# Kernel optimization log

Measured on AMD Instinct MI355X. Metric: run time of the kernel, lower is better.

## Reference

```python
import jax, jax.numpy as jnp
import numpy as np

NUM_HEADS = 12


def setup_inputs() -> dict:
    key = jax.random.key(0)
    k1, k2, k3, k4 = jax.random.split(key, 4)
    B, N, C = 8, 1024, 768
    x = jax.random.normal(k1, (B, N, C), dtype=jnp.float32)
    # nn.Linear(dim, 3*dim, bias=False): weight applied as x @ W, shape [C, 3C]
    w_qkv = jax.random.normal(k2, (C, 3 * C), dtype=jnp.float32) * (C ** -0.5)
    # nn.Linear(dim, dim) with bias
    w_proj = jax.random.normal(k3, (C, C), dtype=jnp.float32) * (C ** -0.5)
    b_proj = jax.random.normal(k4, (C,), dtype=jnp.float32) * 0.01
    return {"x": x, "w_qkv": w_qkv, "w_proj": w_proj, "b_proj": b_proj, "H": 32, "W": 32}


def reference(x, w_qkv, w_proj, b_proj, H, W):
    B, N, C = x.shape
    nh = NUM_HEADS
    hd = C // nh
    scale = hd ** -0.5
    qkv = (x @ w_qkv).reshape(B, N, 3, nh, hd)
    q, k, v = jnp.moveaxis(qkv, 2, 0)  # each [B, N, nh, hd]
    attn = jnp.einsum("bnhd,bmhd->bhnm", q, k) * scale  # [B, nh, N, N]
    attn = jax.nn.softmax(attn, axis=-1)
    out = jnp.einsum("bhnm,bmhd->bnhd", attn, v).reshape(B, N, C)
    return out @ w_proj + b_proj
```

## Files before the change

kernel.cpp:

```cpp
#include <hip/hip_runtime.h>

typedef __bf16 bf16x8 __attribute__((ext_vector_type(8)));
typedef float f32x4 __attribute__((ext_vector_type(4)));
typedef float f32x16 __attribute__((ext_vector_type(16)));
typedef unsigned short u16;
typedef unsigned int u32;
typedef u16 u16x4 __attribute__((ext_vector_type(4)));
typedef u32 u32x4 __attribute__((ext_vector_type(4)));

__device__ __forceinline__ u16 f2bf(float f) {
    union { float f; u32 u; } x{f};
    u32 r = x.u + 0x7FFFu + ((x.u >> 16) & 1u);
    return (u16)(r >> 16);
}

__device__ __forceinline__ float ex2(float x) {
#if __has_builtin(__builtin_amdgcn_exp2f)
    return __builtin_amdgcn_exp2f(x);
#else
    return __expf(x * 0.6931471805599453f);
#endif
}

__device__ __forceinline__ u32 pkbf(float a, float b) {
    union { float f; u32 u; } ca{a}, cb{b};
    return ((ca.u + 0x8000u) >> 16) | (((cb.u + 0x8000u) >> 16) << 16);
}

#define GLD16(g, l)                                                            \
    __builtin_amdgcn_global_load_lds(                                          \
        (const __attribute__((address_space(1))) u32*)(g),                     \
        (__attribute__((address_space(3))) u32*)(l), 16, 0, 0)

__global__ void convert_bf16(const float* __restrict__ src, u16* __restrict__ dst, int n4) {
    int i = blockIdx.x * blockDim.x + threadIdx.x;
    if (i < n4) {
        float4 f = *(const float4*)(src + (size_t)i * 4);
        u16x4 u = { f2bf(f.x), f2bf(f.y), f2bf(f.z), f2bf(f.w) };
        *(u16x4*)(dst + (size_t)i * 4) = u;
    }
}

__global__ __launch_bounds__(256) void prep_weights(
    const float* __restrict__ wq, const float* __restrict__ wp,
    u16* __restrict__ WqT, u16* __restrict__ WpT)
{
    __shared__ u16 tile[32][33];
    int id = blockIdx.x;
    const float* src; u16* dst; int R, C, bx, by;
    if (id < 1728) { src = wq; dst = WqT; R = 768; C = 2304; bx = (id % 72) * 32; by = (id / 72) * 32; }
    else { id -= 1728; src = wp; dst = WpT; R = 768; C = 768; bx = (id % 24) * 32; by = (id / 24) * 32; }
    int x = threadIdx.x & 31, y = threadIdx.x >> 5;
    #pragma unroll
    for (int i = 0; i < 32; i += 8)
        tile[y + i][x] = f2bf(src[(size_t)(by + y + i) * C + bx + x]);
    __syncthreads();
    #pragma unroll
    for (int i = 0; i < 32; i += 8)
        dst[(size_t)(bx + y + i) * R + by + x] = tile[x][y + i];
}

template <int K>
__global__ __launch_bounds__(256) void gemm_qkv(
    const u16* __restrict__ A,
    const u16* __restrict__ Wt,
    u16* __restrict__ QKV,
    u16* __restrict__ Vt,
    float qscale)
{
    __shared__ __align__(16) u16 As[128 * 64];
    __shared__ __align__(16) u16 Bs[128 * 64];

    int tid = threadIdx.x;
    int wave = tid >> 6, lane = tid & 63;
    int quad = lane >> 4, l16 = lane & 15;
    int wm = (wave >> 1) * 64, wn = (wave & 1) * 64;
    int bm = blockIdx.y * 128, bn = blockIdx.x * 128;
    bool vsec = (bn >= 1536);

    f32x4 acc[4][4] = {};

    int srow = lane >> 3;
    int scg = ((lane & 7) ^ srow) * 8;
    const u16* Ap = A + (size_t)(bm + wave * 32 + srow) * K + scg;
    const u16* Bp = Wt + (size_t)(bn + wave * 32 + srow) * K + scg;

    int fg0 = (((0 * 4 + quad) ^ (l16 & 7)) * 8);
    int fg1 = (((1 * 4 + quad) ^ (l16 & 7)) * 8);

    for (int k0 = 0; k0 < K; k0 += 64) {
        #pragma unroll
        for (int j = 0; j < 4; j++) {
            GLD16(Ap + k0 + (size_t)j * 8 * K, &As[(wave * 32 + j * 8) * 64]);
            GLD16(Bp + k0 + (size_t)j * 8 * K, &Bs[(wave * 32 + j * 8) * 64]);
        }
        __syncthreads();

        #pragma unroll
        for (int h = 0; h < 2; h++) {
            int fg = h ? fg1 : fg0;
            bf16x8 af[4], bfr[4];
            #pragma unroll
            for (int i = 0; i < 4; i++) {
                af[i]  = *(const bf16x8*)&As[(wm + i * 16 + l16) * 64 + fg];
                bfr[i] = *(const bf16x8*)&Bs[(wn + i * 16 + l16) * 64 + fg];
            }
            if (!vsec) {
                #pragma unroll
                for (int mi = 0; mi < 4; mi++)
                    #pragma unroll
                    for (int ni = 0; ni < 4; ni++)
                        acc[mi][ni] = __builtin_amdgcn_mfma_f32_16x16x32_bf16(af[mi], bfr[ni], acc[mi][ni], 0, 0, 0);
            } else {
                #pragma unroll
                for (int mi = 0; mi < 4; mi++)
                    #pragma unroll
                    for (int ni = 0; ni < 4; ni++)
                        acc[mi][ni] = __builtin_amdgcn_mfma_f32_16x16x32_bf16(bfr[ni], af[mi], acc[mi][ni], 0, 0, 0);
            }
        }
        __syncthreads();
    }

    if (!vsec) {
        #pragma unroll
        for (int mi = 0; mi < 4; mi++) {
            #pragma unroll
            for (int ni = 0; ni < 4; ni++) {
                #pragma unroll
                for (int rg = 0; rg < 4; rg++) {
                    int row = bm + wm + mi * 16 + quad * 4 + rg;
                    int col = bn + wn + ni * 16 + l16;
                    float sc = (col < 768) ? qscale : 1.0f;
                    QKV[(size_t)row * 2304 + col] = f2bf(acc[mi][ni][rg] * sc);
                }
            }
        }
    } else {
        #pragma unroll
        for (int mi = 0; mi < 4; mi++) {
            #pragma unroll
            for (int ni = 0; ni < 4; ni++) {
                #pragma unroll
                for (int rg = 0; rg < 4; rg++) {
                    int d = (bn - 1536) + wn + ni * 16 + quad * 4 + rg;
                    int ng = bm + wm + mi * 16 + l16;
                    int b = ng >> 10, n = ng & 1023, h = d >> 6;
                    Vt[((size_t)(b * 12 + h) * 64 + (d & 63)) * 1024 + n] = f2bf(acc[mi][ni][rg]);
                }
            }
        }
    }
}

template <int K>
__global__ __launch_bounds__(256) void gemm_proj(
    const u16* __restrict__ A,
    const u16* __restrict__ Bt,
    float* __restrict__ Cp,
    const float* __restrict__ bias,
    int M, int N)
{
    __shared__ __align__(16) u16 As[128 * 64];
    __shared__ __align__(16) u16 Bs[128 * 64];

    int tid = threadIdx.x;
    int wave = tid >> 6, lane = tid & 63;
    int quad = lane >> 4, l16 = lane & 15;
    int wm = (wave >> 1) * 64, wn = (wave & 1) * 64;
    int bm = blockIdx.y * 128, bn = blockIdx.x * 128;

    f32x4 acc[4][4] = {};

    int srow = lane >> 3;
    int scg = ((lane & 7) ^ srow) * 8;
    const u16* Ap = A + (size_t)(bm + wave * 32 + srow) * K + scg;
    const u16* Bp = Bt + (size_t)(bn + wave * 32 + srow) * K + scg;

    int fg0 = (((0 * 4 + quad) ^ (l16 & 7)) * 8);
    int fg1 = (((1 * 4 + quad) ^ (l16 & 7)) * 8);

    for (int k0 = 0; k0 < K; k0 += 64) {
        #pragma unroll
        for (int j = 0; j < 4; j++) {
            GLD16(Ap + k0 + (size_t)j * 8 * K, &As[(wave * 32 + j * 8) * 64]);
            GLD16(Bp + k0 + (size_t)j * 8 * K, &Bs[(wave * 32 + j * 8) * 64]);
        }
        __syncthreads();

        #pragma unroll
        for (int h = 0; h < 2; h++) {
            int fg = h ? fg1 : fg0;
            bf16x8 af[4], bfr[4];
            #pragma unroll
            for (int i = 0; i < 4; i++) {
                af[i]  = *(const bf16x8*)&As[(wm + i * 16 + l16) * 64 + fg];
                bfr[i] = *(const bf16x8*)&Bs[(wn + i * 16 + l16) * 64 + fg];
            }
            #pragma unroll
            for (int mi = 0; mi < 4; mi++)
                #pragma unroll
                for (int ni = 0; ni < 4; ni++)
                    acc[mi][ni] = __builtin_amdgcn_mfma_f32_16x16x32_bf16(af[mi], bfr[ni], acc[mi][ni], 0, 0, 0);
        }
        __syncthreads();
    }

    #pragma unroll
    for (int mi = 0; mi < 4; mi++) {
        #pragma unroll
        for (int ni = 0; ni < 4; ni++) {
            #pragma unroll
            for (int rg = 0; rg < 4; rg++) {
                int row = bm + wm + mi * 16 + quad * 4 + rg;
                int col = bn + wn + ni * 16 + l16;
                Cp[(size_t)row * N + col] = acc[mi][ni][rg] + bias[col];
            }
        }
    }
}

__global__ __launch_bounds__(256, 4) void attn_kernel(
    const u16* __restrict__ qkv,
    const u16* __restrict__ Vt,
    u16* __restrict__ ctx)
{
    __shared__ __align__(16) u16 Ks[2][4096];
    __shared__ __align__(16) u16 Vs[2][4096];

    int qt = blockIdx.x;
    int bh = blockIdx.y;
    int b = bh / 12, h = bh % 12;
    int tid = threadIdx.x;
    int wave = tid >> 6, lane = tid & 63;
    int l32 = lane & 31, half = lane >> 5;

    const u16* qbase = qkv + (size_t)(b * 1024 + qt * 128 + wave * 32 + l32) * 2304 + h * 64;
    bf16x8 qa[4];
    #pragma unroll
    for (int ks = 0; ks < 4; ks++)
        qa[ks] = *(const bf16x8*)(qbase + ks * 16 + half * 8);

    int srow = lane >> 3;
    int scol = (lane & 7) ^ srow;
    const u16* kA = qkv + (size_t)(b * 1024 + wave * 16 + srow) * 2304 + 768 + h * 64 + scol * 8;
    const u16* vA = Vt + ((size_t)bh * 64 + wave * 16 + srow) * 1024 + scol * 8;

    bf16x8 ones;
    #pragma unroll
    for (int j = 0; j < 8; j++) ((u16*)&ones)[j] = 0x3F80;

    f32x16 o0 = {}, o1 = {}, lsum = {};

    int fgo[4];
    #pragma unroll
    for (int ks = 0; ks < 4; ks++)
        fgo[ks] = (((ks * 2 + half) ^ (lane & 7)) * 8);

    {
        GLD16(kA,            &Ks[0][(wave * 2 + 0) * 512]);
        GLD16(kA + 8 * 2304, &Ks[0][(wave * 2 + 1) * 512]);
        GLD16(vA,            &Vs[0][(wave * 2 + 0) * 512]);
        GLD16(vA + 8 * 1024, &Vs[0][(wave * 2 + 1) * 512]);
    }

    #pragma unroll 2
    for (int kt = 0; kt < 16; kt++) {
        int buf = kt & 1;
        __syncthreads();

        if (kt < 15) {
            const u16* k0 = kA + (size_t)(kt + 1) * (64 * 2304);
            const u16* v0 = vA + (size_t)(kt + 1) * 64;
            GLD16(k0,            &Ks[buf ^ 1][(wave * 2 + 0) * 512]);
            GLD16(k0 + 8 * 2304, &Ks[buf ^ 1][(wave * 2 + 1) * 512]);
            GLD16(v0,            &Vs[buf ^ 1][(wave * 2 + 0) * 512]);
            GLD16(v0 + 8 * 1024, &Vs[buf ^ 1][(wave * 2 + 1) * 512]);
        }

        f32x16 st0 = {}, st1 = {};
        #pragma unroll
        for (int ks = 0; ks < 4; ks++) {
            bf16x8 kf0 = *(const bf16x8*)&Ks[buf][(l32)      * 64 + fgo[ks]];
            bf16x8 kf1 = *(const bf16x8*)&Ks[buf][(32 + l32) * 64 + fgo[ks]];
            st0 = __builtin_amdgcn_mfma_f32_32x32x16_bf16(kf0, qa[ks], st0, 0, 0, 0);
            st1 = __builtin_amdgcn_mfma_f32_32x32x16_bf16(kf1, qa[ks], st1, 0, 0, 0);
        }

        bf16x8 pf[4];
        #pragma unroll
        for (int t = 0; t < 2; t++) {
            u32 pk[8];
            #pragma unroll
            for (int g = 0; g < 4; g++) {
                float p0 = ex2(t ? st1[4 * g + 0] : st0[4 * g + 0]);
                float p1 = ex2(t ? st1[4 * g + 1] : st0[4 * g + 1]);
                float p2 = ex2(t ? st1[4 * g + 2] : st0[4 * g + 2]);
                float p3 = ex2(t ? st1[4 * g + 3] : st0[4 * g + 3]);
                pk[2 * g + 0] = pkbf(p0, p1);
                pk[2 * g + 1] = pkbf(p2, p3);
            }
            u32 rA0 = __shfl_xor(half ? pk[0] : pk[2], 32);
            u32 rA1 = __shfl_xor(half ? pk[1] : pk[3], 32);
            u32 rB0 = __shfl_xor(half ? pk[4] : pk[6], 32);
            u32 rB1 = __shfl_xor(half ? pk[5] : pk[7], 32);
            u32x4 f0 = { half ? rA0 : pk[0], half ? rA1 : pk[1],
                         half ? pk[2] : rA0, half ? pk[3] : rA1 };
            u32x4 f1 = { half ? rB0 : pk[4], half ? rB1 : pk[5],
                         half ? pk[6] : rB0, half ? pk[7] : rB1 };
            union { u32x4 u; bf16x8 b; } c0{f0}, c1{f1};
            pf[2 * t + 0] = c0.b;
            pf[2 * t + 1] = c1.b;
        }

        #pragma unroll
        for (int ks = 0; ks < 4; ks++) {
            bf16x8 v0f = *(const bf16x8*)&Vs[buf][(l32)      * 64 + fgo[ks]];
            bf16x8 v1f = *(const bf16x8*)&Vs[buf][(32 + l32) * 64 + fgo[ks]];
            lsum = __builtin_amdgcn_mfma_f32_32x32x16_bf16(pf[ks], ones, lsum, 0, 0, 0);
            o0   = __builtin_amdgcn_mfma_f32_32x32x16_bf16(pf[ks], v0f, o0, 0, 0, 0);
            o1   = __builtin_amdgcn_mfma_f32_32x32x16_bf16(pf[ks], v1f, o1, 0, 0, 0);
        }
    }

    #pragma unroll
    for (int reg = 0; reg < 16; reg++) {
        float inv = 1.0f / lsum[reg];
        int row = (reg & 3) + 8 * (reg >> 2) + 4 * half;
        int qrow = qt * 128 + wave * 32 + row;
        size_t base = (size_t)(b * 1024 + qrow) * 768 + h * 64 + l32;
        ctx[base]      = f2bf(o0[reg] * inv);
        ctx[base + 32] = f2bf(o1[reg] * inv);
    }
}

extern "C" void kernel_launch(void* const* d_in, const int* in_sizes, int n_in,
                              void* d_out, int out_size, void* d_ws, size_t ws_size,
                              hipStream_t stream) {
    const float* x      = (const float*)d_in[0];
    const float* w_qkv  = (const float*)d_in[1];
    const float* w_proj = (const float*)d_in[2];
    const float* b_proj = (const float*)d_in[3];
    float* out = (float*)d_out;

    const int BN = 8192;
    const int C = 768, C3 = 2304;
    const float CE = 0.18033688011112042f;

    u16* Xb      = (u16*)d_ws;
    u16* Wqkv_t  = Xb + (size_t)BN * C;
    u16* Wproj_t = Wqkv_t + (size_t)C3 * C;
    u16* QKV     = Wproj_t + (size_t)C * C;
    u16* Vt      = QKV + (size_t)BN * C3;
    u16* Ctx     = Vt + (size_t)96 * 64 * 1024;

    convert_bf16<<<(BN * C / 4 + 255) / 256, 256, 0, stream>>>(x, Xb, BN * C / 4);
    prep_weights<<<2304, 256, 0, stream>>>(w_qkv, w_proj, Wqkv_t, Wproj_t);

    gemm_qkv<768><<<dim3(C3 / 128, BN / 128), 256, 0, stream>>>(
        Xb, Wqkv_t, QKV, Vt, CE);

    attn_kernel<<<dim3(8, 96), 256, 0, stream>>>(QKV, Vt, Ctx);

    gemm_proj<768><<<dim3(C / 128, BN / 128), 256, 0, stream>>>(
        Ctx, Wproj_t, out, b_proj, BN, C);
}
```

Baseline: 194.7 us.

## Triple-buffer QKV GEMM with 256x128 tiles, 32x32 MFMA and tile swizzle

The QKV projection GEMM now uses 512-thread blocks computing 256x128 tiles. Global-to-LDS loads are triple-buffered in dynamic shared memory, with partial vmcnt waits and raw barriers replacing the full syncthreads around each k-step. It also switches to 32x32x16 bf16 MFMA, raises wave priority during the MFMA section, and remaps block IDs so neighbouring blocks share tiles in L2. The projection GEMM also moves to 32x32 MFMA. The cost is 144KB of LDS per block, which limits occupancy to one block per CU.

After: 196.3 us. Within noise of the previous version (+0.8%).

```diff
diff --git a/kernel.cpp b/kernel.cpp
--- a/kernel.cpp
+++ b/kernel.cpp
@@ -60,98 +60,122 @@
         dst[(size_t)(bx + y + i) * R + by + x] = tile[x][y + i];
 }
 
+#define MFMA32 __builtin_amdgcn_mfma_f32_32x32x16_bf16
+
+#define STG(tt)                                                                 \
+    {                                                                           \
+        u16* ab_ = &lds[((tt) % 3) * 24576];                                    \
+        GLD16(Ap + (tt) * 64 + (size_t)0 * 8 * K, &ab_[(wave * 32 + 0)  * 64]); \
+        GLD16(Ap + (tt) * 64 + (size_t)1 * 8 * K, &ab_[(wave * 32 + 8)  * 64]); \
+        GLD16(Ap + (tt) * 64 + (size_t)2 * 8 * K, &ab_[(wave * 32 + 16) * 64]); \
+        GLD16(Ap + (tt) * 64 + (size_t)3 * 8 * K, &ab_[(wave * 32 + 24) * 64]); \
+        GLD16(Bp + (tt) * 64 + (size_t)0 * 8 * K, &ab_[16384 + (wave * 16 + 0) * 64]); \
+        GLD16(Bp + (tt) * 64 + (size_t)1 * 8 * K, &ab_[16384 + (wave * 16 + 8) * 64]); \
+    }
+
 template <int K>
-__global__ __launch_bounds__(256) void gemm_qkv(
+__global__ __launch_bounds__(512, 1) void gemm_qkv(
     const u16* __restrict__ A,
     const u16* __restrict__ Wt,
     u16* __restrict__ QKV,
     u16* __restrict__ Vt,
     float qscale)
 {
-    __shared__ __align__(16) u16 As[128 * 64];
-    __shared__ __align__(16) u16 Bs[128 * 64];
+    extern __shared__ __align__(16) u16 lds[];
+
+    constexpr int NT = K / 64;
 
     int tid = threadIdx.x;
     int wave = tid >> 6, lane = tid & 63;
-    int quad = lane >> 4, l16 = lane & 15;
+    int l31 = lane & 31, half = lane >> 5;
     int wm = (wave >> 1) * 64, wn = (wave & 1) * 64;
-    int bm = blockIdx.y * 128, bn = blockIdx.x * 128;
+
+    int id = blockIdx.x;
+    int lin = (id & 7) * 72 + (id >> 3);
+    int bm = (lin / 18) * 256;
+    int bn = (lin % 18) * 128;
     bool vsec = (bn >= 1536);
 
-    f32x4 acc[4][4] = {};
+    f32x16 acc[2][2] = {};
 
     int srow = lane >> 3;
     int scg = ((lane & 7) ^ srow) * 8;
-    const u16* Ap = A + (size_t)(bm + wave * 32 + srow) * K + scg;
-    const u16* Bp = Wt + (size_t)(bn + wave * 32 + srow) * K + scg;
-
-    int fg0 = (((0 * 4 + quad) ^ (l16 & 7)) * 8);
-    int fg1 = (((1 * 4 + quad) ^ (l16 & 7)) * 8);
-
-    for (int k0 = 0; k0 < K; k0 += 64) {
-        #pragma unroll
-        for (int j = 0; j < 4; j++) {
-            GLD16(Ap + k0 + (size_t)j * 8 * K, &As[(wave * 32 + j * 8) * 64]);
-            GLD16(Bp + k0 + (size_t)j * 8 * K, &Bs[(wave * 32 + j * 8) * 64]);
-        }
-        __syncthreads();
-
-        #pragma unroll
-        for (int h = 0; h < 2; h++) {
-            int fg = h ? fg1 : fg0;
-            bf16x8 af[4], bfr[4];
+    const u16* Ap = A  + (size_t)(bm + wave * 32 + srow) * K + scg;
+    const u16* Bp = Wt + (size_t)(bn + wave * 16 + srow) * K + scg;
+
+    STG(0);
+    STG(1);
+    asm volatile("s_waitcnt vmcnt(6)" ::: "memory");
+    __builtin_amdgcn_s_barrier();
+
+    #pragma unroll 3
+    for (int t = 0; t < NT; ++t) {
+        const u16* Ab = &lds[(t % 3) * 24576];
+        const u16* Bb = Ab + 16384;
+
+        if (t + 2 < NT) STG(t + 2);
+
+        __builtin_amdgcn_s_setprio(1);
+        #pragma unroll
+        for (int kc = 0; kc < 4; ++kc) {
+            int g = ((kc * 2 + half) ^ (l31 & 7)) * 8;
+            bf16x8 a0 = *(const bf16x8*)&Ab[(wm +  0 + l31) * 64 + g];
+            bf16x8 a1 = *(const bf16x8*)&Ab[(wm + 32 + l31) * 64 + g];
+            bf16x8 b0 = *(const bf16x8*)&Bb[(wn +  0 + l31) * 64 + g];
+            bf16x8 b1 = *(const bf16x8*)&Bb[(wn + 32 + l31) * 64 + g];
+            if (!vsec) {
+                acc[0][0] = MFMA32(a0, b0, acc[0][0], 0, 0, 0);
+                acc[0][1] = MFMA32(a0, b1, acc[0][1], 0, 0, 0);
+                acc[1][0] = MFMA32(a1, b0, acc[1][0], 0, 0, 0);
+                acc[1][1] = MFMA32(a1, b1, acc[1][1], 0, 0, 0);
+            } else {
+                acc[0][0] = MFMA32(b0, a0, acc[0][0], 0, 0, 0);
+                acc[0][1] = MFMA32(b1, a0, acc[0][1], 0, 0, 0);
+                acc[1][0] = MFMA32(b0, a1, acc[1][0], 0, 0, 0);
+                acc[1][1] = MFMA32(b1, a1, acc[1][1], 0, 0, 0);
+            }
+        }
+        __builtin_amdgcn_s_setprio(0);
+
+        if (t + 1 < NT) {
+            if (t + 2 < NT) { asm volatile("s_waitcnt vmcnt(6)" ::: "memory"); }
+            else            { asm volatile("s_waitcnt vmcnt(0)" ::: "memory"); }
+            __builtin_amdgcn_s_barrier();
+        }
+    }
+
+    if (!vsec) {
+        float sc = (bn < 768) ? qscale : 1.0f;
+        #pragma unroll
+        for (int mi = 0; mi < 2; mi++) {
             #pragma unroll
-            for (int i = 0; i < 4; i++) {
-                af[i]  = *(const bf16x8*)&As[(wm + i * 16 + l16) * 64 + fg];
-                bfr[i] = *(const bf16x8*)&Bs[(wn + i * 16 + l16) * 64 + fg];
-            }
-            if (!vsec) {
+            for (int ni = 0; ni < 2; ni++) {
                 #pragma unroll
-                for (int mi = 0; mi < 4; mi++)
-                    #pragma unroll
-                    for (int ni = 0; ni < 4; ni++)
-                        acc[mi][ni] = __builtin_amdgcn_mfma_f32_16x16x32_bf16(af[mi], bfr[ni], acc[mi][ni], 0, 0, 0);
-            } else {
+                for (int r = 0; r < 16; r++) {
+                    int row = bm + wm + mi * 32 + (r & 3) + 8 * (r >> 2) + 4 * half;
+                    int col = bn + wn + ni * 32 + l31;
+                    QKV[(size_t)row * 2304 + col] = f2bf(acc[mi][ni][r] * sc);
+                }
+            }
+        }
+    } else {
+        #pragma unroll
+        for (int mi = 0; mi < 2; mi++) {
+            #pragma unroll
+            for (int ni = 0; ni < 2; ni++) {
                 #pragma unroll
-                for (int mi = 0; mi < 4; mi++)
-                    #pragma unroll
-                    for (int ni = 0; ni < 4; ni++)
-                        acc[mi][ni] = __builtin_amdgcn_mfma_f32_16x16x32_bf16(bfr[ni], af[mi], acc[mi][ni], 0, 0, 0);
-            }
-        }
-        __syncthreads();
-    }
-
-    if (!vsec) {
-        #pragma unroll
-        for (int mi = 0; mi < 4; mi++) {
-            #pragma unroll
-            for (int ni = 0; ni < 4; ni++) {
-                #pragma unroll
-                for (int rg = 0; rg < 4; rg++) {
-                    int row = bm + wm + mi * 16 + quad * 4 + rg;
-                    int col = bn + wn + ni * 16 + l16;
-                    float sc = (col < 768) ? qscale : 1.0f;
-                    QKV[(size_t)row * 2304 + col] = f2bf(acc[mi][ni][rg] * sc);
+                for (int r = 0; r < 16; r++) {
+                    int d = (bn - 1536) + wn + ni * 32 + (r & 3) + 8 * (r >> 2) + 4 * half;
+                    int ng = bm + wm + mi * 32 + l31;
+                    int b = ng >> 10, n = ng & 1023, h = d >> 6;
+                    Vt[((size_t)(b * 12 + h) * 64 + (d & 63)) * 1024 + n] = f2bf(acc[mi][ni][r]);
                 }
             }
         }
-    } else {
-        #pragma unroll
-        for (int mi = 0; mi < 4; mi++) {
-            #pragma unroll
-            for (int ni = 0; ni < 4; ni++) {
-                #pragma unroll
-                for (int rg = 0; rg < 4; rg++) {
-                    int d = (bn - 1536) + wn + ni * 16 + quad * 4 + rg;
-                    int ng = bm + wm + mi * 16 + l16;
-                    int b = ng >> 10, n = ng & 1023, h = d >> 6;
-                    Vt[((size_t)(b * 12 + h) * 64 + (d & 63)) * 1024 + n] = f2bf(acc[mi][ni][rg]);
-                }
-            }
-        }
-    }
-}
+    }
+}
+
+#undef STG
 
 template <int K>
 __global__ __launch_bounds__(256) void gemm_proj(
@@ -166,20 +190,17 @@
 
     int tid = threadIdx.x;
     int wave = tid >> 6, lane = tid & 63;
-    int quad = lane >> 4, l16 = lane & 15;
+    int l31 = lane & 31, half = lane >> 5;
     int wm = (wave >> 1) * 64, wn = (wave & 1) * 64;
     int bm = blockIdx.y * 128, bn = blockIdx.x * 128;
 
-    f32x4 acc[4][4] = {};
+    f32x16 acc[2][2] = {};
 
     int srow = lane >> 3;
     int scg = ((lane & 7) ^ srow) * 8;
     const u16* Ap = A + (size_t)(bm + wave * 32 + srow) * K + scg;
     const u16* Bp = Bt + (size_t)(bn + wave * 32 + srow) * K + scg;
 
-    int fg0 = (((0 * 4 + quad) ^ (l16 & 7)) * 8);
-    int fg1 = (((1 * 4 + quad) ^ (l16 & 7)) * 8);
-
     for (int k0 = 0; k0 < K; k0 += 64) {
         #pragma unroll
         for (int j = 0; j < 4; j++) {
@@ -189,32 +210,29 @@
         __syncthreads();
 
         #pragma unroll
-        for (int h = 0; h < 2; h++) {
-            int fg = h ? fg1 : fg0;
-            bf16x8 af[4], bfr[4];
+        for (int kc = 0; kc < 4; ++kc) {
+            int g = ((kc * 2 + half) ^ (l31 & 7)) * 8;
+            bf16x8 a0 = *(const bf16x8*)&As[(wm +  0 + l31) * 64 + g];
+            bf16x8 a1 = *(const bf16x8*)&As[(wm + 32 + l31) * 64 + g];
+            bf16x8 b0 = *(const bf16x8*)&Bs[(wn +  0 + l31) * 64 + g];
+            bf16x8 b1 = *(const bf16x8*)&Bs[(wn + 32 + l31) * 64 + g];
+            acc[0][0] = MFMA32(a0, b0, acc[0][0], 0, 0, 0);
+            acc[0][1] = MFMA32(a0, b1, acc[0][1], 0, 0, 0);
+            acc[1][0] = MFMA32(a1, b0, acc[1][0], 0, 0, 0);
+            acc[1][1] = MFMA32(a1, b1, acc[1][1], 0, 0, 0);
+        }
+        __syncthreads();
+    }
+
+    #pragma unroll
+    for (int mi = 0; mi < 2; mi++) {
+        #pragma unroll
+        for (int ni = 0; ni < 2; ni++) {
             #pragma unroll
-            for (int i = 0; i < 4; i++) {
-                af[i]  = *(const bf16x8*)&As[(wm + i * 16 + l16) * 64 + fg];
-                bfr[i] = *(const bf16x8*)&Bs[(wn + i * 16 + l16) * 64 + fg];
-            }
-            #pragma unroll
-            for (int mi = 0; mi < 4; mi++)
-                #pragma unroll
-                for (int ni = 0; ni < 4; ni++)
-                    acc[mi][ni] = __builtin_amdgcn_mfma_f32_16x16x32_bf16(af[mi], bfr[ni], acc[mi][ni], 0, 0, 0);
-        }
-        __syncthreads();
-    }
-
-    #pragma unroll
-    for (int mi = 0; mi < 4; mi++) {
-        #pragma unroll
-        for (int ni = 0; ni < 4; ni++) {
-            #pragma unroll
-            for (int rg = 0; rg < 4; rg++) {
-                int row = bm + wm + mi * 16 + quad * 4 + rg;
-                int col = bn + wn + ni * 16 + l16;
-                Cp[(size_t)row * N + col] = acc[mi][ni][rg] + bias[col];
+            for (int r = 0; r < 16; r++) {
+                int row = bm + wm + mi * 32 + (r & 3) + 8 * (r >> 2) + 4 * half;
+                int col = bn + wn + ni * 32 + l31;
+                Cp[(size_t)row * N + col] = acc[mi][ni][r] + bias[col];
             }
         }
     }
@@ -354,11 +372,17 @@
     u16* Vt      = QKV + (size_t)BN * C3;
     u16* Ctx     = Vt + (size_t)96 * 64 * 1024;
 
+    static bool s_attr = false;
+    if (!s_attr) {
+        (void)hipFuncSetAttribute((const void*)gemm_qkv<768>,
+                                  hipFuncAttributeMaxDynamicSharedMemorySize, 147456);
+        s_attr = true;
+    }
+
     convert_bf16<<<(BN * C / 4 + 255) / 256, 256, 0, stream>>>(x, Xb, BN * C / 4);
     prep_weights<<<2304, 256, 0, stream>>>(w_qkv, w_proj, Wqkv_t, Wproj_t);
 
-    gemm_qkv<768><<<dim3(C3 / 128, BN / 128), 256, 0, stream>>>(
-        Xb, Wqkv_t, QKV, Vt, CE);
+    gemm_qkv<768><<<576, 512, 147456, stream>>>(Xb, Wqkv_t, QKV, Vt, CE);
 
     attn_kernel<<<dim3(8, 96), 256, 0, stream>>>(QKV, Vt, Ctx);
 
```

## Triple-buffer QKV GEMM with 256x128 tiles, 8 waves and swizzled block order

Applied to the files above, without the earlier changes.

Rewrites the QKV projection GEMM to use 512-thread blocks computing 256x128 tiles, with a three-stage LDS ring buffer in dynamic shared memory so global loads for tile t+2 overlap MFMA work on tile t. Loads are split into two half-phases interleaved with the two K-halves, using explicit vmcnt waits, raw barriers and s_setprio to favour MFMA issue. Blocks are remapped with an XCD-aware linear ordering to improve L2 locality. This costs much more LDS per block (one block per CU) and more complex synchronisation.

Measured after the change: 197.0 us. No clear change (+1.2%).

```diff
diff --git a/kernel.cpp b/kernel.cpp
--- a/kernel.cpp
+++ b/kernel.cpp
@@ -60,69 +60,128 @@
         dst[(size_t)(bx + y + i) * R + by + x] = tile[x][y + i];
 }
 
+#define MFMA16 __builtin_amdgcn_mfma_f32_16x16x32_bf16
+
+#define STG_P0(tt)                                                              \
+    {                                                                           \
+        u16* ab_ = &lds[((tt) % 3) * 24576];                                    \
+        GLD16(Ap + (tt) * 64 + (size_t)0 * 8 * K, &ab_[(wave * 32 + 0)  * 64]); \
+        GLD16(Ap + (tt) * 64 + (size_t)1 * 8 * K, &ab_[(wave * 32 + 8)  * 64]); \
+        GLD16(Ap + (tt) * 64 + (size_t)2 * 8 * K, &ab_[(wave * 32 + 16) * 64]); \
+    }
+#define STG_P1(tt)                                                              \
+    {                                                                           \
+        u16* ab_ = &lds[((tt) % 3) * 24576];                                    \
+        GLD16(Ap + (tt) * 64 + (size_t)3 * 8 * K, &ab_[(wave * 32 + 24) * 64]); \
+        GLD16(Bp + (tt) * 64 + (size_t)0 * 8 * K, &ab_[16384 + (wave * 16 + 0) * 64]); \
+        GLD16(Bp + (tt) * 64 + (size_t)1 * 8 * K, &ab_[16384 + (wave * 16 + 8) * 64]); \
+    }
+
 template <int K>
-__global__ __launch_bounds__(256) void gemm_qkv(
+__global__ __launch_bounds__(512, 1) void gemm_qkv(
     const u16* __restrict__ A,
     const u16* __restrict__ Wt,
     u16* __restrict__ QKV,
     u16* __restrict__ Vt,
     float qscale)
 {
-    __shared__ __align__(16) u16 As[128 * 64];
-    __shared__ __align__(16) u16 Bs[128 * 64];
+    extern __shared__ __align__(16) u16 lds[];
+
+    constexpr int NT = K / 64;
 
     int tid = threadIdx.x;
     int wave = tid >> 6, lane = tid & 63;
     int quad = lane >> 4, l16 = lane & 15;
-    int wm = (wave >> 1) * 64, wn = (wave & 1) * 64;
-    int bm = blockIdx.y * 128, bn = blockIdx.x * 128;
+    int wm = (wave >> 1) * 64;
+    int wn = (wave & 1) * 64;
+
+    int id = blockIdx.x;
+    int lin = (id & 7) * 72 + (id >> 3);
+    int bm = (lin / 18) * 256;
+    int bn = (lin % 18) * 128;
     bool vsec = (bn >= 1536);
 
     f32x4 acc[4][4] = {};
 
     int srow = lane >> 3;
     int scg = ((lane & 7) ^ srow) * 8;
-    const u16* Ap = A + (size_t)(bm + wave * 32 + srow) * K + scg;
-    const u16* Bp = Wt + (size_t)(bn + wave * 32 + srow) * K + scg;
-
-    int fg0 = (((0 * 4 + quad) ^ (l16 & 7)) * 8);
-    int fg1 = (((1 * 4 + quad) ^ (l16 & 7)) * 8);
-
-    for (int k0 = 0; k0 < K; k0 += 64) {
-        #pragma unroll
-        for (int j = 0; j < 4; j++) {
-            GLD16(Ap + k0 + (size_t)j * 8 * K, &As[(wave * 32 + j * 8) * 64]);
-            GLD16(Bp + k0 + (size_t)j * 8 * K, &Bs[(wave * 32 + j * 8) * 64]);
-        }
-        __syncthreads();
-
-        #pragma unroll
-        for (int h = 0; h < 2; h++) {
-            int fg = h ? fg1 : fg0;
+    const u16* Ap = A  + (size_t)(bm + wave * 32 + srow) * K + scg;
+    const u16* Bp = Wt + (size_t)(bn + wave * 16 + srow) * K + scg;
+
+    int fg0 = ((0 * 4 + quad) ^ (l16 & 7)) * 8;
+    int fg1 = ((1 * 4 + quad) ^ (l16 & 7)) * 8;
+
+    STG_P0(0); STG_P1(0);
+    STG_P0(1); STG_P1(1);
+    asm volatile("s_waitcnt vmcnt(6)" ::: "memory");
+    __builtin_amdgcn_s_barrier();
+
+    #pragma unroll 3
+    for (int t = 0; t < NT; ++t) {
+        const u16* Ab = &lds[(t % 3) * 24576];
+        const u16* Bb = Ab + 16384;
+
+        {
             bf16x8 af[4], bfr[4];
             #pragma unroll
             for (int i = 0; i < 4; i++) {
-                af[i]  = *(const bf16x8*)&As[(wm + i * 16 + l16) * 64 + fg];
-                bfr[i] = *(const bf16x8*)&Bs[(wn + i * 16 + l16) * 64 + fg];
-            }
+                af[i]  = *(const bf16x8*)&Ab[(wm + i * 16 + l16) * 64 + fg0];
+                bfr[i] = *(const bf16x8*)&Bb[(wn + i * 16 + l16) * 64 + fg0];
+            }
+            if (t + 2 < NT) STG_P0(t + 2);
+            __builtin_amdgcn_s_barrier();
+            __builtin_amdgcn_s_setprio(1);
             if (!vsec) {
                 #pragma unroll
                 for (int mi = 0; mi < 4; mi++)
                     #pragma unroll
                     for (int ni = 0; ni < 4; ni++)
-                        acc[mi][ni] = __builtin_amdgcn_mfma_f32_16x16x32_bf16(af[mi], bfr[ni], acc[mi][ni], 0, 0, 0);
+                        acc[mi][ni] = MFMA16(af[mi], bfr[ni], acc[mi][ni], 0, 0, 0);
             } else {
                 #pragma unroll
                 for (int mi = 0; mi < 4; mi++)
                     #pragma unroll
                     for (int ni = 0; ni < 4; ni++)
-                        acc[mi][ni] = __builtin_amdgcn_mfma_f32_16x16x32_bf16(bfr[ni], af[mi], acc[mi][ni], 0, 0, 0);
-            }
-        }
-        __syncthreads();
+                        acc[mi][ni] = MFMA16(bfr[ni], af[mi], acc[mi][ni], 0, 0, 0);
+            }
+            __builtin_amdgcn_s_setprio(0);
+            __builtin_amdgcn_s_barrier();
+        }
+
+        {
+            bf16x8 af[4], bfr[4];
+            #pragma unroll
+            for (int i = 0; i < 4; i++) {
+                af[i]  = *(const bf16x8*)&Ab[(wm + i * 16 + l16) * 64 + fg1];
+                bfr[i] = *(const bf16x8*)&Bb[(wn + i * 16 + l16) * 64 + fg1];
+            }
+            if (t + 2 < NT) STG_P1(t + 2);
+            __builtin_amdgcn_s_barrier();
+            __builtin_amdgcn_s_setprio(1);
+            if (!vsec) {
+                #pragma unroll
+                for (int mi = 0; mi < 4; mi++)
+                    #pragma unroll
+                    for (int ni = 0; ni < 4; ni++)
+                        acc[mi][ni] = MFMA16(af[mi], bfr[ni], acc[mi][ni], 0, 0, 0);
+            } else {
+                #pragma unroll
+                for (int mi = 0; mi < 4; mi++)
+                    #pragma unroll
+                    for (int ni = 0; ni < 4; ni++)
+                        acc[mi][ni] = MFMA16(bfr[ni], af[mi], acc[mi][ni], 0, 0, 0);
+            }
+            __builtin_amdgcn_s_setprio(0);
+            if (t + 1 < NT) {
+                if (t + 2 < NT) { asm volatile("s_waitcnt vmcnt(6)" ::: "memory"); }
+                else            { asm volatile("s_waitcnt vmcnt(0)" ::: "memory"); }
+            }
+            __builtin_amdgcn_s_barrier();
+        }
     }
 
     if (!vsec) {
+        float sc = (bn < 768) ? qscale : 1.0f;
         #pragma unroll
         for (int mi = 0; mi < 4; mi++) {
             #pragma unroll
@@ -131,7 +190,6 @@
                 for (int rg = 0; rg < 4; rg++) {
                     int row = bm + wm + mi * 16 + quad * 4 + rg;
                     int col = bn + wn + ni * 16 + l16;
-                    float sc = (col < 768) ? qscale : 1.0f;
                     QKV[(size_t)row * 2304 + col] = f2bf(acc[mi][ni][rg] * sc);
                 }
             }
@@ -152,6 +210,9 @@
         }
     }
 }
+
+#undef STG_P0
+#undef STG_P1
 
 template <int K>
 __global__ __launch_bounds__(256) void gemm_proj(
@@ -354,11 +415,17 @@
     u16* Vt      = QKV + (size_t)BN * C3;
     u16* Ctx     = Vt + (size_t)96 * 64 * 1024;
 
+    static bool s_attr = false;
+    if (!s_attr) {
+        (void)hipFuncSetAttribute((const void*)gemm_qkv<768>,
+                                  hipFuncAttributeMaxDynamicSharedMemorySize, 147456);
+        s_attr = true;
+    }
+
     convert_bf16<<<(BN * C / 4 + 255) / 256, 256, 0, stream>>>(x, Xb, BN * C / 4);
     prep_weights<<<2304, 256, 0, stream>>>(w_qkv, w_proj, Wqkv_t, Wproj_t);
 
-    gemm_qkv<768><<<dim3(C3 / 128, BN / 128), 256, 0, stream>>>(
-        Xb, Wqkv_t, QKV, Vt, CE);
+    gemm_qkv<768><<<576, 512, 147456, stream>>>(Xb, Wqkv_t, QKV, Vt, CE);
 
     attn_kernel<<<dim3(8, 96), 256, 0, stream>>>(QKV, Vt, Ctx);
 
```
